# Optimization experiments

Hardware: AMD Instinct MI355X
Metric: run time of the kernel (lower is better)

Reference implementation:

```python
import jax, jax.numpy as jnp
import numpy as np

N, K, D = 65536, 1024, 256


def setup_inputs() -> dict:
    key = jax.random.key(0)
    k1, k2 = jax.random.split(key)
    e = jax.random.normal(k1, (N, D), dtype=jnp.float32)
    # module inits codebook uniform in [-1/K, 1/K]
    weight = jax.random.uniform(k2, (K, D), dtype=jnp.float32,
                                minval=-1.0 / K, maxval=1.0 / K)
    return {"e": e, "weight": weight}


def reference(e, weight):
    distances = (jnp.sum(e * e, axis=1, keepdims=True)
                 - 2.0 * jnp.matmul(e, weight.T)
                 + jnp.sum(weight * weight, axis=1))
    encoding_indices = jnp.argmin(distances, axis=1)            # [N]
    # one-hot @ weight is just a gather
    quantized = weight[encoding_indices]                        # [N, D]
    commitment_loss = jnp.mean((jax.lax.stop_gradient(quantized) - e) ** 2)
    counts = jnp.zeros((K,), dtype=jnp.float32).at[encoding_indices].add(1.0)
    codebook_usage = counts.max() / counts.sum()
    # straight-through estimator
    quantized = e + jax.lax.stop_gradient(quantized - e)
    return quantized, encoding_indices, commitment_loss, codebook_usage
```

## Files before the change

kernel.cpp:

```cpp
#include <hip/hip_runtime.h>

typedef __attribute__((ext_vector_type(8))) short short8;
typedef __attribute__((ext_vector_type(4))) float floatx4;

#define N_ROWS 65536
#define K_CB   1024
#define D_DIM  256

#define TAU 4.0e-4f
#define BLINE 520
#define PRS 260

#define OFF_WN     262144
#define OFF_FIXCNT 266240
#define OFF_HIST   266496
#define OFF_IDX    270592
#define OFF_LIST   532736
#define OFF_PART   794880
#define OFF_WFRAG  827392
#define OFF_KEYS   1351680
#define OFF_WT     1875968

__device__ __forceinline__ float pw128_sq(const float4* p) {
#pragma clang fp contract(off)
    float4 q0 = p[0], q1 = p[1];
    float r0 = q0.x * q0.x, r1 = q0.y * q0.y, r2 = q0.z * q0.z, r3 = q0.w * q0.w;
    float r4 = q1.x * q1.x, r5 = q1.y * q1.y, r6 = q1.z * q1.z, r7 = q1.w * q1.w;
    for (int i = 1; i < 16; ++i) {
        float4 u0 = p[2 * i], u1 = p[2 * i + 1];
        r0 = r0 + u0.x * u0.x; r1 = r1 + u0.y * u0.y;
        r2 = r2 + u0.z * u0.z; r3 = r3 + u0.w * u0.w;
        r4 = r4 + u1.x * u1.x; r5 = r5 + u1.y * u1.y;
        r6 = r6 + u1.z * u1.z; r7 = r7 + u1.w * u1.w;
    }
    return ((r0 + r1) + (r2 + r3)) + ((r4 + r5) + (r6 + r7));
}
__device__ __forceinline__ float rownorm_np(const float* row) {
#pragma clang fp contract(off)
    float s0 = pw128_sq((const float4*)row);
    float s1 = pw128_sq((const float4*)(row + 128));
    return s0 + s1;
}
__device__ __forceinline__ float np_dist(float A, float m, float Ck) {
#pragma clang fp contract(off)
    float Bv = 2.0f * m;
    float t  = A - Bv;
    return t + Ck;
}
__device__ __forceinline__ unsigned short bf16_rne(float x) {
    unsigned u = __float_as_uint(x);
    unsigned r = u + 0x7fff + ((u >> 16) & 1);
    return (unsigned short)(r >> 16);
}
__device__ __forceinline__ unsigned long long dist_key(float d, int idx) {
    unsigned u = __float_as_uint(d);
    unsigned k32 = u ^ (((unsigned)((int)u >> 31)) | 0x80000000u);
    return ((unsigned long long)k32 << 32) | (unsigned)idx;
}

__global__ __launch_bounds__(256) void k_prep(
        const float* __restrict__ wg,
        float* __restrict__ wn,
        unsigned short* __restrict__ wfrag, float* __restrict__ wt) {
    __shared__ __align__(16) float es[32 * PRS];
    const int tid = threadIdx.x;
    const int bx  = blockIdx.x;
    if (bx < 4) {
        int row = bx * 256 + tid;
        wn[row] = rownorm_np(wg + (size_t)row * D_DIM);
    } else if (bx < 132) {
        int t = (bx - 4) * 256 + tid;
        int col = t >> 5, kc = t & 31;
        const float4* src = (const float4*)(wg + (size_t)col * D_DIM + kc * 8);
        float4 v0 = src[0], v1 = src[1];
        const float a[8] = {v0.x, v0.y, v0.z, v0.w, v1.x, v1.y, v1.z, v1.w};
        short8 h;
        #pragma unroll
        for (int i = 0; i < 8; ++i) h[i] = (short)bf16_rne(a[i]);
        *(short8*)(wfrag + ((size_t)kc * 1024 + col) * 8) = h;
    } else {
        float (*tw)[PRS] = (float(*)[PRS])es;
        const int cb = bx - 132;
        const int c0 = cb * 32;
        #pragma unroll
        for (int it = 0; it < 8; ++it) {
            int idx = it * 256 + tid;
            int code = idx >> 6, f4 = idx & 63;
            *(float4*)&tw[code][f4 * 4] =
                *(const float4*)(wg + (size_t)(c0 + code) * D_DIM + f4 * 4);
        }
        __syncthreads();
        const int j = tid & 31, dg = tid >> 5;
        #pragma unroll
        for (int dd = 0; dd < 32; ++dd) {
            int d = dd * 8 + dg;
            wt[(size_t)d * K_CB + c0 + j] = tw[j][d];
        }
    }
}

__global__ __launch_bounds__(256, 2) void k_dist(
        const float* __restrict__ eg, const unsigned short* __restrict__ wfrag,
        const float* __restrict__ wn,
        int* __restrict__ idx_ws, int* __restrict__ fixlist, int* __restrict__ fixcnt) {
    __shared__ __align__(16) unsigned short Bs[2][32 * BLINE];
    __shared__ float wnS[K_CB];
    const int tid  = threadIdx.x;
    const int lane = tid & 63;
    const int wv   = tid >> 6;
    const int q    = lane >> 4;
    const int m15  = lane & 15;
    const int waveRow = blockIdx.x * 128 + wv * 32;

    #pragma unroll
    for (int i = 0; i < 4; ++i) wnS[tid + i * 256] = wn[tid + i * 256];

    float* ef = (float*)&Bs[0][0];
    short8 afh0[8], afh1[8];
    #pragma unroll
    for (int mt = 0; mt < 2; ++mt) {
        #pragma unroll
        for (int t = 0; t < 16; ++t) {
            int slot = wv * 16 + t;
            const float* src = eg + (size_t)(waveRow + mt * 16 + t) * D_DIM + lane * 4;
            __builtin_amdgcn_global_load_lds(
                (const __attribute__((address_space(1))) unsigned int*)src,
                (__attribute__((address_space(3))) unsigned int*)&ef[slot * PRS],
                16, 0, 0);
        }
        __syncthreads();
        const float* rowp = &ef[(wv * 16 + m15) * PRS + q * 8];
        #pragma unroll
        for (int win = 0; win < 8; ++win) {
            float4 x0 = *(const float4*)(rowp + win * 32);
            float4 x1 = *(const float4*)(rowp + win * 32 + 4);
            const float a[8] = {x0.x, x0.y, x0.z, x0.w, x1.x, x1.y, x1.z, x1.w};
            short8 h;
            #pragma unroll
            for (int i = 0; i < 8; ++i) h[i] = (short)bf16_rne(a[i]);
            if (mt == 0) afh0[win] = h; else afh1[win] = h;
        }
        __syncthreads();
    }

    float best[8], sec[8];
    int bidx[8];
    #pragma unroll
    for (int s = 0; s < 8; ++s) { best[s] = 3.4e38f; sec[s] = 3.4e38f; bidx[s] = 0; }

    #pragma unroll
    for (int t = 0; t < 8; ++t) {
        int L = wv * 8 + t;
        const unsigned short* src = wfrag + ((size_t)L * 1024) * 8 + lane * 8;
        __builtin_amdgcn_global_load_lds(
            (const __attribute__((address_space(1))) unsigned int*)src,
            (__attribute__((address_space(3))) unsigned int*)&Bs[0][L * BLINE],
            16, 0, 0);
    }
    __syncthreads();

    for (int cb = 0; cb < 16; ++cb) {
        const int p = cb & 1;
        if (cb < 15) {
            #pragma unroll
            for (int t = 0; t < 8; ++t) {
                int L = wv * 8 + t;
                const unsigned short* src =
                    wfrag + ((size_t)L * 1024 + (cb + 1) * 64) * 8 + lane * 8;
                __builtin_amdgcn_global_load_lds(
                    (const __attribute__((address_space(1))) unsigned int*)src,
                    (__attribute__((address_space(3))) unsigned int*)&Bs[p ^ 1][L * BLINE],
                    16, 0, 0);
            }
        }
        floatx4 acc[2][4];
        #pragma unroll
        for (int mt = 0; mt < 2; ++mt)
            #pragma unroll
            for (int nt = 0; nt < 4; ++nt)
                acc[mt][nt] = (floatx4){0.f, 0.f, 0.f, 0.f};
        #pragma unroll
        for (int win = 0; win < 8; ++win) {
            int kc = win * 4 + q;
            #pragma unroll
            for (int nt = 0; nt < 4; ++nt) {
                short8 bfh = *(short8*)&Bs[p][kc * BLINE + (nt * 16 + m15) * 8];
                acc[0][nt] = __builtin_amdgcn_mfma_f32_16x16x32_bf16(afh0[win], bfh, acc[0][nt], 0, 0, 0);
                acc[1][nt] = __builtin_amdgcn_mfma_f32_16x16x32_bf16(afh1[win], bfh, acc[1][nt], 0, 0, 0);
            }
        }
        #pragma unroll
        for (int nt = 0; nt < 4; ++nt) {
            int col = cb * 64 + nt * 16 + m15;
            float Ck = wnS[col];
            #pragma unroll
            for (int reg = 0; reg < 4; ++reg) {
                float d0 = __builtin_fmaf(-2.0f, acc[0][nt][reg], Ck);
                bool lt0 = d0 < best[reg];
                sec[reg]  = __builtin_amdgcn_fmed3f(d0, best[reg], sec[reg]);
                best[reg] = fminf(d0, best[reg]);
                bidx[reg] = lt0 ? col : bidx[reg];
                float d1 = __builtin_fmaf(-2.0f, acc[1][nt][reg], Ck);
                int s1 = 4 + reg;
                bool lt1 = d1 < best[s1];
                sec[s1]  = __builtin_amdgcn_fmed3f(d1, best[s1], sec[s1]);
                best[s1] = fminf(d1, best[s1]);
                bidx[s1] = lt1 ? col : bidx[s1];
            }
        }
        __syncthreads();
    }

    #pragma unroll
    for (int s = 0; s < 8; ++s) {
        float b = best[s], se = sec[s];
        int ix = bidx[s];
        #pragma unroll
        for (int m = 1; m < 16; m <<= 1) {
            float bo = __shfl_xor(b, m, 64);
            float so = __shfl_xor(se, m, 64);
            int   io = __shfl_xor(ix, m, 64);
            float ns = fminf(fminf(se, so), fmaxf(b, bo));
            if (bo < b || (bo == b && io < ix)) { b = bo; ix = io; }
            se = ns;
        }
        if (m15 == 0) {
            int row = waveRow + (s >> 2) * 16 + q * 4 + (s & 3);
            idx_ws[row] = ix;
            if (se - b < TAU) {
                int p = atomicAdd(fixcnt, 1);
                fixlist[p] = row;
            }
        }
    }
}

#define FG_ROWS 8
__global__ __launch_bounds__(256) void k_fixup(
        const float* __restrict__ eg, const float* __restrict__ wg,
        const float* __restrict__ wt, const float* __restrict__ wnorm,
        const int* __restrict__ fixlist, const int* __restrict__ fixcnt,
        unsigned long long* __restrict__ keys) {
    __shared__ __align__(16) float xs[FG_ROWS][D_DIM];
    __shared__ float AnS[FG_ROWS];
    const int tid  = threadIdx.x;
    const int lane = tid & 63;
    const int cnt = *fixcnt;
    if (cnt == 0) return;
    const int ngroups = (cnt + FG_ROWS - 1) / FG_ROWS;
    const int ntiles  = ngroups * 2;
    const int rowg = tid >> 7;
    const int cg   = tid & 127;
    for (int t = blockIdx.x; t < ntiles; t += gridDim.x) {
        const int g     = t >> 1;
        const int chunk = t & 1;
        __syncthreads();
        int rows[FG_ROWS];
        #pragma unroll
        for (int i = 0; i < FG_ROWS; ++i) {
            int j = g * FG_ROWS + i;
            rows[i] = fixlist[j < cnt ? j : cnt - 1];
        }
        #pragma unroll
        for (int i = 0; i < FG_ROWS; ++i)
            xs[i][tid] = eg[(size_t)rows[i] * D_DIM + tid];
        __syncthreads();

        if (tid < 16) {
            int row = tid >> 1, half = tid & 1;
            float sN = pw128_sq((const float4*)&xs[row][half * 128]);
            float so = __shfl_xor(sN, 1, 64);
            if (half == 0) AnS[row] = sN + so;
        }

        const int c0 = chunk * 512 + cg * 4;
        float Cw[4];
        #pragma unroll
        for (int c = 0; c < 4; ++c) Cw[c] = wnorm[c0 + c];

        float s[4][4];
        #pragma unroll
        for (int r = 0; r < 4; ++r)
            #pragma unroll
            for (int c = 0; c < 4; ++c) s[r][c] = 0.f;

        #pragma unroll 2
        for (int d = 0; d < D_DIM; d += 2) {
            float4 wa = *(const float4*)(wt + (size_t)d * K_CB + c0);
            float4 wb = *(const float4*)(wt + (size_t)(d + 1) * K_CB + c0);
            #pragma unroll
            for (int r = 0; r < 4; ++r) {
                float2 e2 = *(const float2*)&xs[rowg * 4 + r][d];
                s[r][0] += e2.x * wa.x + e2.y * wb.x;
                s[r][1] += e2.x * wa.y + e2.y * wb.y;
                s[r][2] += e2.x * wa.z + e2.y * wb.z;
                s[r][3] += e2.x * wa.w + e2.y * wb.w;
            }
        }
        __syncthreads();

        #pragma unroll
        for (int r = 0; r < 4; ++r) {
            const int R = rowg * 4 + r;
            float An = AnS[R];
            unsigned long long kb = 0xFFFFFFFFFFFFFFFFull, ks = 0xFFFFFFFFFFFFFFFFull;
            #pragma unroll
            for (int c = 0; c < 4; ++c) {
                float dq = np_dist(An, s[r][c], Cw[c]);
                unsigned long long kk = dist_key(dq, c0 + c);
                if (kk < kb) { ks = kb; kb = kk; }
                else if (kk < ks) { ks = kk; }
            }
            #pragma unroll
            for (int m = 1; m < 64; m <<= 1) {
                unsigned long long ko = __shfl_xor(kb, m, 64);
                unsigned long long so = __shfl_xor(ks, m, 64);
                if (ko < kb) { ks = (so < kb) ? so : kb; kb = ko; }
                else         { ks = (ko < ks) ? ko : ks; }
            }
            int cand = (int)((lane < 32 ? kb : ks) & 0xFFFFFFFFull);
            const float* wrow = wg + (size_t)cand * D_DIM + (lane & 31) * 8;
            const float* erow = &xs[R][(lane & 31) * 8];
            double sm = 0.0;
            #pragma unroll
            for (int jj = 0; jj < 8; ++jj)
                sm += (double)erow[jj] * (double)wrow[jj];
            #pragma unroll
            for (int m = 1; m < 32; m <<= 1) sm += __shfl_xor(sm, m, 64);
            double smo = __shfl_xor(sm, 32, 64);
            if (lane == 0) {
                int i0 = (int)(kb & 0xFFFFFFFFull);
                int i1 = (int)(ks & 0xFFFFFFFFull);
                float d0 = np_dist(An, (float)sm,  wnorm[i0]);
                float d1 = np_dist(An, (float)smo, wnorm[i1]);
                unsigned long long k0 = dist_key(d0, i0);
                unsigned long long k1 = dist_key(d1, i1);
                unsigned long long kf = k0 < k1 ? k0 : k1;
                int j = g * FG_ROWS + R;
                if (j < cnt) atomicMin(&keys[j], kf);
            }
        }
    }
}

__global__ void k_fixscatter(const int* __restrict__ fixlist, const int* __restrict__ fixcnt,
                             const unsigned long long* __restrict__ keys,
                             int* __restrict__ idx_ws) {
    const int cnt = *fixcnt;
    for (int j = blockIdx.x * blockDim.x + threadIdx.x; j < cnt;
         j += gridDim.x * blockDim.x)
        idx_ws[fixlist[j]] = (int)(keys[j] & 0xFFFFFFFFull);
}

__global__ void k_final(const float* __restrict__ eg, const float* __restrict__ wg,
                        const int* __restrict__ idx_ws, float* __restrict__ qout,
                        float* __restrict__ iout, int* __restrict__ hist,
                        double* __restrict__ partials) {
    const int tid  = threadIdx.x;
    const int sub  = tid >> 6;
    const int lane = tid & 63;
    const int rowBase = blockIdx.x * 16;
    double acc = 0.0;
    #pragma unroll
    for (int g = 0; g < 4; ++g) {
        int row = rowBase + g * 4 + sub;
        int k = idx_ws[row];
        float4 ev = ((const float4*)(eg + (size_t)row * D_DIM))[lane];
        float4 wv = ((const float4*)(wg + (size_t)k   * D_DIM))[lane];
        float dx = wv.x - ev.x, dy = wv.y - ev.y, dz = wv.z - ev.z, dw = wv.w - ev.w;
        float4 qv = {ev.x + dx, ev.y + dy, ev.z + dz, ev.w + dw};
        ((float4*)(qout + (size_t)row * D_DIM))[lane] = qv;
        acc += (double)(dx * dx) + (double)(dy * dy)
             + (double)(dz * dz) + (double)(dw * dw);
        if (lane == 0) {
            iout[row] = (float)k;
            atomicAdd(&hist[k], 1);
        }
    }
    __shared__ double red[256];
    red[tid] = acc;
    __syncthreads();
    for (int st = 128; st > 0; st >>= 1) {
        if (tid < st) red[tid] += red[tid + st];
        __syncthreads();
    }
    if (tid == 0) partials[blockIdx.x] = red[0];
}

__global__ void k_scalars(const int* __restrict__ hist, const double* __restrict__ partials,
                          float* __restrict__ sout) {
    const int tid = threadIdx.x;
    double s = 0.0;
    for (int j = tid; j < N_ROWS / 16; j += 256) s += partials[j];
    int m = 0;
    for (int j = tid; j < K_CB; j += 256) m = max(m, hist[j]);
    __shared__ double rs[256];
    __shared__ int    rm[256];
    rs[tid] = s; rm[tid] = m;
    __syncthreads();
    for (int st = 128; st > 0; st >>= 1) {
        if (tid < st) { rs[tid] += rs[tid + st]; rm[tid] = max(rm[tid], rm[tid + st]); }
        __syncthreads();
    }
    if (tid == 0) {
        sout[0] = (float)(rs[0] / (double)((size_t)N_ROWS * D_DIM));
        sout[1] = (float)rm[0] / 65536.0f;
    }
}

extern "C" void kernel_launch(void* const* d_in, const int* in_sizes, int n_in,
                              void* d_out, int out_size, void* d_ws, size_t ws_size,
                              hipStream_t stream) {
    const float* e = (const float*)d_in[0];
    const float* w = (const float*)d_in[1];
    float* out  = (float*)d_out;
    float* qout = out;
    float* iout = out + (size_t)N_ROWS * D_DIM;
    float* sout = iout + N_ROWS;

    char* ws = (char*)d_ws;
    float*  wn       = (float*) (ws + OFF_WN);
    int*    fixcnt   = (int*)   (ws + OFF_FIXCNT);
    int*    hist     = (int*)   (ws + OFF_HIST);
    int*    idxp     = (int*)   (ws + OFF_IDX);
    int*    list     = (int*)   (ws + OFF_LIST);
    double* partials = (double*)(ws + OFF_PART);
    unsigned short* wfrag = (unsigned short*)(ws + OFF_WFRAG);
    unsigned long long* keys = (unsigned long long*)(ws + OFF_KEYS);
    float*  wt       = (float*) (ws + OFF_WT);

    hipMemsetAsync(ws + OFF_FIXCNT, 0, 4352, stream);
    hipMemsetAsync(ws + OFF_KEYS, 0xFF, 524288, stream);

    hipLaunchKernelGGL(k_prep,       dim3(164),         dim3(256), 0, stream, w, wn, wfrag, wt);
    hipLaunchKernelGGL(k_dist,       dim3(512),         dim3(256), 0, stream, e, wfrag, wn, idxp, list, fixcnt);
    hipLaunchKernelGGL(k_fixup,      dim3(2048),        dim3(256), 0, stream, e, w, wt, wn, list, fixcnt, keys);
    hipLaunchKernelGGL(k_fixscatter, dim3(64),          dim3(256), 0, stream, list, fixcnt, keys, idxp);
    hipLaunchKernelGGL(k_final,      dim3(N_ROWS / 16), dim3(256), 0, stream, e, w, idxp, qout, iout, hist, partials);
    hipLaunchKernelGGL(k_scalars,    dim3(1),           dim3(256), 0, stream, hist, partials, sout);
}
```

Measured before the change: 295.9 us.

## Shrink k_dist to 128-thread single-buffered blocks for higher occupancy

Halves the k_dist block to two waves covering 64 rows and doubles the grid. The codebook LDS tile goes from double-buffered with prefetch to a single buffer loaded synchronously each chunk. The intent is to cut LDS per block so more blocks fit per CU and latency is hidden by other blocks instead of in-block prefetch. In exchange, each block loses its load/compute overlap, and the codebook fragments are streamed twice as many times overall because each block now serves fewer rows.

New measurement: 300.4 us. No clear change (+1.5%).

```diff
diff --git a/kernel.cpp b/kernel.cpp
--- a/kernel.cpp
+++ b/kernel.cpp
@@ -99,46 +99,51 @@
     }
 }
 
-__global__ __launch_bounds__(256, 2) void k_dist(
+__global__ __launch_bounds__(128) void k_dist(
         const float* __restrict__ eg, const unsigned short* __restrict__ wfrag,
         const float* __restrict__ wn,
         int* __restrict__ idx_ws, int* __restrict__ fixlist, int* __restrict__ fixcnt) {
-    __shared__ __align__(16) unsigned short Bs[2][32 * BLINE];
+    __shared__ __align__(16) unsigned short Bs[32 * BLINE];
     __shared__ float wnS[K_CB];
     const int tid  = threadIdx.x;
     const int lane = tid & 63;
     const int wv   = tid >> 6;
     const int q    = lane >> 4;
     const int m15  = lane & 15;
-    const int waveRow = blockIdx.x * 128 + wv * 32;
+    const int waveRow = blockIdx.x * 64 + wv * 32;
 
     #pragma unroll
-    for (int i = 0; i < 4; ++i) wnS[tid + i * 256] = wn[tid + i * 256];
-
-    float* ef = (float*)&Bs[0][0];
+    for (int i = 0; i < 8; ++i) wnS[tid + i * 128] = wn[tid + i * 128];
+
+    float* ef = (float*)&Bs[0];
     short8 afh0[8], afh1[8];
     #pragma unroll
-    for (int mt = 0; mt < 2; ++mt) {
+    for (int round = 0; round < 2; ++round) {
         #pragma unroll
         for (int t = 0; t < 16; ++t) {
-            int slot = wv * 16 + t;
-            const float* src = eg + (size_t)(waveRow + mt * 16 + t) * D_DIM + lane * 4;
+            int line = wv * 16 + t;
+            const float* src = eg + (size_t)(blockIdx.x * 64 + round * 32 + line) * D_DIM + lane * 4;
             __builtin_amdgcn_global_load_lds(
                 (const __attribute__((address_space(1))) unsigned int*)src,
-                (__attribute__((address_space(3))) unsigned int*)&ef[slot * PRS],
+                (__attribute__((address_space(3))) unsigned int*)&ef[line * PRS],
                 16, 0, 0);
         }
         __syncthreads();
-        const float* rowp = &ef[(wv * 16 + m15) * PRS + q * 8];
-        #pragma unroll
-        for (int win = 0; win < 8; ++win) {
-            float4 x0 = *(const float4*)(rowp + win * 32);
-            float4 x1 = *(const float4*)(rowp + win * 32 + 4);
-            const float a[8] = {x0.x, x0.y, x0.z, x0.w, x1.x, x1.y, x1.z, x1.w};
-            short8 h;
-            #pragma unroll
-            for (int i = 0; i < 8; ++i) h[i] = (short)bf16_rne(a[i]);
-            if (mt == 0) afh0[win] = h; else afh1[win] = h;
+        if (wv == round) {
+            #pragma unroll
+            for (int mt = 0; mt < 2; ++mt) {
+                const float* rowp = &ef[(mt * 16 + m15) * PRS + q * 8];
+                #pragma unroll
+                for (int win = 0; win < 8; ++win) {
+                    float4 x0 = *(const float4*)(rowp + win * 32);
+                    float4 x1 = *(const float4*)(rowp + win * 32 + 4);
+                    const float a[8] = {x0.x, x0.y, x0.z, x0.w, x1.x, x1.y, x1.z, x1.w};
+                    short8 h;
+                    #pragma unroll
+                    for (int i = 0; i < 8; ++i) h[i] = (short)bf16_rne(a[i]);
+                    if (mt == 0) afh0[win] = h; else afh1[win] = h;
+                }
+            }
         }
         __syncthreads();
     }
@@ -148,31 +153,18 @@
     #pragma unroll
     for (int s = 0; s < 8; ++s) { best[s] = 3.4e38f; sec[s] = 3.4e38f; bidx[s] = 0; }
 
-    #pragma unroll
-    for (int t = 0; t < 8; ++t) {
-        int L = wv * 8 + t;
-        const unsigned short* src = wfrag + ((size_t)L * 1024) * 8 + lane * 8;
-        __builtin_amdgcn_global_load_lds(
-            (const __attribute__((address_space(1))) unsigned int*)src,
-            (__attribute__((address_space(3))) unsigned int*)&Bs[0][L * BLINE],
-            16, 0, 0);
-    }
-    __syncthreads();
-
     for (int cb = 0; cb < 16; ++cb) {
-        const int p = cb & 1;
-        if (cb < 15) {
-            #pragma unroll
-            for (int t = 0; t < 8; ++t) {
-                int L = wv * 8 + t;
-                const unsigned short* src =
-                    wfrag + ((size_t)L * 1024 + (cb + 1) * 64) * 8 + lane * 8;
-                __builtin_amdgcn_global_load_lds(
-                    (const __attribute__((address_space(1))) unsigned int*)src,
-                    (__attribute__((address_space(3))) unsigned int*)&Bs[p ^ 1][L * BLINE],
-                    16, 0, 0);
-            }
-        }
+        #pragma unroll
+        for (int t = 0; t < 16; ++t) {
+            int L = wv * 16 + t;
+            const unsigned short* src = wfrag + ((size_t)L * 1024 + cb * 64) * 8 + lane * 8;
+            __builtin_amdgcn_global_load_lds(
+                (const __attribute__((address_space(1))) unsigned int*)src,
+                (__attribute__((address_space(3))) unsigned int*)&Bs[L * BLINE],
+                16, 0, 0);
+        }
+        __syncthreads();
+
         floatx4 acc[2][4];
         #pragma unroll
         for (int mt = 0; mt < 2; ++mt)
@@ -184,7 +176,7 @@
             int kc = win * 4 + q;
             #pragma unroll
             for (int nt = 0; nt < 4; ++nt) {
-                short8 bfh = *(short8*)&Bs[p][kc * BLINE + (nt * 16 + m15) * 8];
+                short8 bfh = *(short8*)&Bs[kc * BLINE + (nt * 16 + m15) * 8];
                 acc[0][nt] = __builtin_amdgcn_mfma_f32_16x16x32_bf16(afh0[win], bfh, acc[0][nt], 0, 0, 0);
                 acc[1][nt] = __builtin_amdgcn_mfma_f32_16x16x32_bf16(afh1[win], bfh, acc[1][nt], 0, 0, 0);
             }
@@ -433,7 +425,7 @@
     hipMemsetAsync(ws + OFF_KEYS, 0xFF, 524288, stream);
 
     hipLaunchKernelGGL(k_prep,       dim3(164),         dim3(256), 0, stream, w, wn, wfrag, wt);
-    hipLaunchKernelGGL(k_dist,       dim3(512),         dim3(256), 0, stream, e, wfrag, wn, idxp, list, fixcnt);
+    hipLaunchKernelGGL(k_dist,       dim3(1024),        dim3(128), 0, stream, e, wfrag, wn, idxp, list, fixcnt);
     hipLaunchKernelGGL(k_fixup,      dim3(2048),        dim3(256), 0, stream, e, w, wt, wn, list, fixcnt, keys);
     hipLaunchKernelGGL(k_fixscatter, dim3(64),          dim3(256), 0, stream, list, fixcnt, keys, idxp);
     hipLaunchKernelGGL(k_final,      dim3(N_ROWS / 16), dim3(256), 0, stream, e, w, idxp, qout, iout, hist, partials);
```
